# Kernel optimization log

Measured on AMD Instinct MI355X. Metric: run time of the kernel, lower is better.

## Reference

```python
import jax, jax.numpy as jnp
import numpy as np

B, S, D, H = 4, 1024, 768, 12
E = D // H  # head dim = 64

def setup_inputs() -> dict:
    key = jax.random.key(0)
    ks = jax.random.split(key, 8)
    sd = 1.0 / np.sqrt(D)
    return {
        'x':    jax.random.normal(ks[0], (B, S, D), jnp.float32),
        'Wqkv': jax.random.normal(ks[1], (3 * D, D), jnp.float32) * sd,
        'Wl':   jax.random.normal(ks[2], (H, H), jnp.float32) * (1.0 / np.sqrt(H)),
        'bl':   jax.random.normal(ks[3], (H,), jnp.float32) * 0.01,
        'Ww':   jax.random.normal(ks[4], (H, H), jnp.float32) * (1.0 / np.sqrt(H)),
        'bw':   jax.random.normal(ks[5], (H,), jnp.float32) * 0.01,
        'Wp':   jax.random.normal(ks[6], (D, D), jnp.float32) * sd,
        'bp':   jax.random.normal(ks[7], (D,), jnp.float32) * 0.01,
    }

def reference(x, Wqkv, Wl, bl, Ww, bw, Wp, bp):
    # qkv: [B,S,3D] -> [B,S,3,H,E] -> q,k,v each [B,H,S,E]
    qkv = jnp.einsum('bsd,fd->bsf', x, Wqkv)
    qkv = qkv.reshape(B, S, 3, H, E).transpose(2, 0, 3, 1, 4)
    q, k, v = qkv[0], qkv[1], qkv[2]
    # NOTE: source computes but never applies the 1/sqrt(E) scale; stay faithful.
    attn = jnp.einsum('bhqe,bhke->bhqk', q, k)            # [B,H,S,S]
    # talking-heads mix before softmax: Linear over head axis
    attn = jnp.einsum('bhqk,gh->bgqk', attn, Wl) + bl[None, :, None, None]
    attn = jax.nn.softmax(attn, axis=-1)
    # talking-heads mix after softmax
    attn = jnp.einsum('bhqk,gh->bgqk', attn, Ww) + bw[None, :, None, None]
    out = jnp.einsum('bhqk,bhke->bhqe', attn, v)          # [B,H,S,E]
    out = out.transpose(0, 2, 1, 3).reshape(B, S, D)      # b h s e -> b s (h e)
    return jnp.einsum('bsd,fd->bsf', out, Wp) + bp
```

## Files before the change

### kernel.cpp

```cpp
#include <hip/hip_runtime.h>
#include <math.h>


typedef _Float16 f16;
typedef __attribute__((ext_vector_type(8))) _Float16 f16x8;
typedef __attribute__((ext_vector_type(4))) _Float16 f16x4;
typedef __attribute__((ext_vector_type(2))) _Float16 f16x2;
typedef __attribute__((ext_vector_type(4))) float f32x4;
typedef __attribute__((ext_vector_type(2))) float f32x2;
typedef __attribute__((ext_vector_type(2))) unsigned u32x2;
typedef unsigned short u16;

__device__ __forceinline__ u16 f2h(float f) {
  f16 h = (f16)f;
  return __builtin_bit_cast(u16, h);
}
__device__ __forceinline__ unsigned pk2h(float a, float b) {
  return __builtin_bit_cast(unsigned, __builtin_amdgcn_cvt_pkrtz(a, b));
}
__device__ __forceinline__ float exp2_native(float x) {
  float r;
  asm("v_exp_f32 %0, %1" : "=v"(r) : "v"(x));
  return r;
}

__device__ __forceinline__ void async16(const void* g, void* l) {
  __builtin_amdgcn_global_load_lds(
      (const __attribute__((address_space(1))) unsigned int*)g,
      (__attribute__((address_space(3))) unsigned int*)l, 16, 0, 0);
}

#define MFMA_F16(a, b, c) __builtin_amdgcn_mfma_f32_16x16x32_f16((a), (b), (c), 0, 0, 0)
#define MFMA16(a, b, c) __builtin_amdgcn_mfma_f32_16x16x16f16((a), (b), (c), 0, 0, 0)

__global__ __launch_bounds__(256) void k_prep(const float* __restrict__ x,
                                              const float* __restrict__ Wqkv,
                                              const float* __restrict__ Wp,
                                              u16* __restrict__ xh,
                                              u16* __restrict__ wh,
                                              u16* __restrict__ wph) {
  const int blk = blockIdx.x, t = threadIdx.x;
  if (blk < 3072) {
    int i = blk * 256 + t;
    float4 v = ((const float4*)x)[i];
    ((ushort4*)xh)[i] = make_ushort4(f2h(v.x), f2h(v.y), f2h(v.z), f2h(v.w));
  } else if (blk < 4800) {
    int i = (blk - 3072) * 256 + t;
    float4 v = ((const float4*)Wqkv)[i];
    ((ushort4*)wh)[i] = make_ushort4(f2h(v.x), f2h(v.y), f2h(v.z), f2h(v.w));
  } else {
    int i = (blk - 4800) * 256 + t;
    float4 v = ((const float4*)Wp)[i];
    ((ushort4*)wph)[i] = make_ushort4(f2h(v.x), f2h(v.y), f2h(v.z), f2h(v.w));
  }
}

__global__ __launch_bounds__(256) void k_qkv(const u16* __restrict__ Axh,
                                             const u16* __restrict__ Bwh,
                                             u16* __restrict__ qkf,
                                             u16* __restrict__ vbuf) {
  __shared__ u16 smem[16384];
  u16* As = smem;
  u16* Bs = smem + 4096;
  const int t = threadIdx.x, lane = t & 63, wave = t >> 6;
  const int wm = wave >> 1, wn = wave & 1;
  const int quad = lane >> 4, l16 = lane & 15;
  const int pid = blockIdx.x;
  const int group = pid / 144;
  const int rem = pid - group * 144;
  const int m0 = (group * 8 + (rem & 7)) * 128;
  const int n0 = (rem >> 3) * 128;
  const bool vblk = (n0 >= 1536);
  const int srow = t >> 2, sch = (t & 3) * 8;
  f32x4 acc[4][4];
#pragma unroll
  for (int i = 0; i < 4; ++i)
#pragma unroll
    for (int j = 0; j < 4; ++j) acc[i][j] = (f32x4){0.f, 0.f, 0.f, 0.f};
  for (int k0 = 0; k0 < 768; k0 += 32) {
    const size_t ga = (size_t)(m0 + srow) * 768 + k0 + sch;
    const size_t gb = (size_t)(n0 + srow) * 768 + k0 + sch;
    __syncthreads();
    async16(Axh + ga, &As[t * 8]);
    async16(Axh + ga + (size_t)64 * 768, &As[2048 + t * 8]);
    async16(Bwh + gb, &Bs[t * 8]);
    async16(Bwh + gb + (size_t)64 * 768, &Bs[2048 + t * 8]);
    __syncthreads();
    f16x8 af[4], bfr[4];
#pragma unroll
    for (int i = 0; i < 4; ++i) af[i] = *(const f16x8*)&As[(wm * 64 + i * 16 + l16) * 32 + quad * 8];
#pragma unroll
    for (int j = 0; j < 4; ++j) bfr[j] = *(const f16x8*)&Bs[(wn * 64 + j * 16 + l16) * 32 + quad * 8];
#pragma unroll
    for (int i = 0; i < 4; ++i)
#pragma unroll
      for (int j = 0; j < 4; ++j) acc[i][j] = MFMA_F16(af[i], bfr[j], acc[i][j]);
  }
  __syncthreads();
  u16* T = smem;
#pragma unroll
  for (int i = 0; i < 4; ++i)
#pragma unroll
    for (int j = 0; j < 4; ++j)
#pragma unroll
      for (int r = 0; r < 4; ++r) {
        const int row = wm * 64 + i * 16 + quad * 4 + r;
        const int col = wn * 64 + j * 16 + l16;
        T[row * 128 + (col ^ ((row & 7) << 4))] = f2h(acc[i][j][r]);
      }
  __syncthreads();
  const int row = t >> 1, halfc = (t & 1) * 64;
  const int sw = (row & 7) << 4;
  u16* dst = vblk ? (vbuf + (size_t)(m0 + row) * 768 + (n0 - 1536) + halfc)
                  : (qkf + (size_t)(m0 + row) * 1536 + n0 + halfc);
#pragma unroll
  for (int c = 0; c < 64; c += 8)
    *(uint4*)(dst + c) = *(const uint4*)&T[row * 128 + ((halfc + c) ^ sw)];
}

__global__ __launch_bounds__(256) void k_qk(const u16* __restrict__ qkf,
                                            u16* __restrict__ scbuf) {
  __shared__ u16 smem[17408];
  u16* As = smem;
  u16* Bs = smem + 8192;
  const int t = threadIdx.x, lane = t & 63, wave = t >> 6;
  const int wm = wave >> 1, wn = wave & 1;
  const int quad = lane >> 4, l16 = lane & 15;
  const int bh = blockIdx.z, b = bh / 12, h = bh % 12;
  const int m0 = blockIdx.y * 128, n0 = blockIdx.x * 128;
#pragma unroll
  for (int i = 0; i < 4; ++i) {
    const int ci = i * 256 + t;
    const int row = ci >> 3, ch = ci & 7;
    const int chs = ch ^ (row & 7);
    async16(qkf + (size_t)(b * 1024 + m0 + row) * 1536 + h * 64 + chs * 8, &As[ci * 8]);
    async16(qkf + (size_t)(b * 1024 + n0 + row) * 1536 + 768 + h * 64 + chs * 8, &Bs[ci * 8]);
  }
  f32x4 acc[4][4];
#pragma unroll
  for (int i = 0; i < 4; ++i)
#pragma unroll
    for (int j = 0; j < 4; ++j) acc[i][j] = (f32x4){0.f, 0.f, 0.f, 0.f};
  __syncthreads();
  const int sx = l16 & 7;
#pragma unroll
  for (int k0 = 0; k0 < 2; ++k0) {
    const int fch = ((k0 * 4 + quad) ^ sx) * 8;
    f16x8 af[4], bfr[4];
#pragma unroll
    for (int i = 0; i < 4; ++i) af[i] = *(const f16x8*)&As[(wm * 64 + i * 16 + l16) * 64 + fch];
#pragma unroll
    for (int j = 0; j < 4; ++j) bfr[j] = *(const f16x8*)&Bs[(wn * 64 + j * 16 + l16) * 64 + fch];
#pragma unroll
    for (int i = 0; i < 4; ++i)
#pragma unroll
      for (int j = 0; j < 4; ++j) acc[i][j] = MFMA_F16(af[i], bfr[j], acc[i][j]);
  }
  __syncthreads();
  u16* T = smem;
#pragma unroll
  for (int i = 0; i < 4; ++i)
#pragma unroll
    for (int j = 0; j < 4; ++j)
#pragma unroll
      for (int r = 0; r < 4; ++r) {
        const int row = wm * 64 + i * 16 + quad * 4 + r;
        const int col = wn * 64 + j * 16 + l16;
        T[row * 136 + col] = f2h(acc[i][j][r]);
      }
  __syncthreads();
  const int row = t >> 1, halfc = (t & 1) * 64;
  u16* dst = scbuf + ((size_t)(b * 1024 + m0 + row) * 12 + h) * 1024 + n0 + halfc;
#pragma unroll
  for (int c = 0; c < 64; c += 8)
    *(uint4*)(dst + c) = *(const uint4*)&T[row * 136 + halfc + c];
}

__global__ __launch_bounds__(256) void k_mix(u16* __restrict__ scbuf,
                                             const float* __restrict__ Wl,
                                             const float* __restrict__ bl,
                                             const float* __restrict__ Ww,
                                             const float* __restrict__ bw) {
  __shared__ float red[4][16];
  const int t = threadIdx.x, lane = t & 63, wave = t >> 6;
  const int quad = lane >> 4, l16 = lane & 15;
  const int bq = blockIdx.x, b = bq >> 10, q = bq & 1023;
  const size_t qslab = (size_t)(b * 1024 + q) * 12288;
  const float L2E = 1.44269504088896f;
  const bool actA = (quad < 3);
  f16x4 Awl = (f16x4){0, 0, 0, 0}, Aww = (f16x4){0, 0, 0, 0};
  if (actA && l16 < 12) {
    const float4 wl4 = *(const float4*)&Wl[l16 * 12 + quad * 4];
    const float4 ww4 = *(const float4*)&Ww[l16 * 12 + quad * 4];
    Awl[0] = (f16)(wl4.x * L2E); Awl[1] = (f16)(wl4.y * L2E);
    Awl[2] = (f16)(wl4.z * L2E); Awl[3] = (f16)(wl4.w * L2E);
    Aww[0] = (f16)ww4.x; Aww[1] = (f16)ww4.y; Aww[2] = (f16)ww4.z; Aww[3] = (f16)ww4.w;
  }
  float blv[4], bwv[4];
#pragma unroll
  for (int r = 0; r < 4; ++r) {
    blv[r] = actA ? (bl[quad * 4 + r] - 16.f) * L2E : 0.f;
    bwv[r] = actA ? bw[quad * 4 + r] : 0.f;
  }
  const u16* const Sg = scbuf + qslab + (size_t)(quad * 4) * 1024 + l16;
  float Ev[16][4];
  float a0 = 0.f, a1 = 0.f, a2 = 0.f, a3 = 0.f;
#pragma unroll
  for (int i = 0; i < 16; ++i) {
    const int kb = (wave * 16 + i) * 16;
    f16x4 B1 = (f16x4){0, 0, 0, 0};
    if (actA) {
#pragma unroll
      for (int j = 0; j < 4; ++j) B1[j] = __builtin_bit_cast(f16, Sg[j * 1024 + kb]);
    }
    f32x4 c1 = (f32x4){blv[0], blv[1], blv[2], blv[3]};
    c1 = MFMA16(Awl, B1, c1);
    const float e0 = exp2_native(c1[0]), e1 = exp2_native(c1[1]);
    const float e2 = exp2_native(c1[2]), e3 = exp2_native(c1[3]);
    Ev[i][0] = e0; Ev[i][1] = e1; Ev[i][2] = e2; Ev[i][3] = e3;
    a0 += e0; a1 += e1; a2 += e2; a3 += e3;
  }
#pragma unroll
  for (int m = 1; m <= 8; m <<= 1) {
    a0 += __shfl_xor(a0, m); a1 += __shfl_xor(a1, m);
    a2 += __shfl_xor(a2, m); a3 += __shfl_xor(a3, m);
  }
  if (l16 == 0) {
    red[wave][quad * 4 + 0] = a0; red[wave][quad * 4 + 1] = a1;
    red[wave][quad * 4 + 2] = a2; red[wave][quad * 4 + 3] = a3;
  }
  __syncthreads();
  float dinv[4];
#pragma unroll
  for (int r = 0; r < 4; ++r) {
    const int g = quad * 4 + r;
    dinv[r] = 1.0f / (red[0][g] + red[1][g] + red[2][g] + red[3][g]);
  }
  u16* const outp = scbuf + qslab + (size_t)quad * 4096 + l16;
#pragma unroll
  for (int i = 0; i < 16; ++i) {
    const int kb = (wave * 16 + i) * 16;
    const unsigned lo = pk2h(Ev[i][0] * dinv[0], Ev[i][1] * dinv[1]);
    const unsigned hi = pk2h(Ev[i][2] * dinv[2], Ev[i][3] * dinv[3]);
    u32x2 pw = {lo, hi};
    const f16x4 Pf = __builtin_bit_cast(f16x4, pw);
    f32x4 c2 = (f32x4){bwv[0], bwv[1], bwv[2], bwv[3]};
    c2 = MFMA16(Aww, Pf, c2);
    if (actA) {
#pragma unroll
      for (int r = 0; r < 4; ++r) outp[r * 1024 + kb] = f2h(c2[r]);
    }
  }
}

__global__ __launch_bounds__(256) void k_pv(const u16* __restrict__ probs,
                                            const u16* __restrict__ vbuf,
                                            u16* __restrict__ ctx) {
  __shared__ u16 As[4096];
  __shared__ u16 Bs[64 * 40];
  const int t = threadIdx.x, lane = t & 63, wave = t >> 6;
  const int wm = wave >> 1, wn = wave & 1;
  const int quad = lane >> 4, l16 = lane & 15;
  const int bh = blockIdx.y, b = bh / 12, h = bh % 12;
  const int m0 = blockIdx.x * 128;
  const int srow = t >> 2, sch = (t & 3) * 8;
  const int ev = t & 63, s8 = (t >> 6) * 8;
  f32x4 acc[4][2];
#pragma unroll
  for (int i = 0; i < 4; ++i)
#pragma unroll
    for (int j = 0; j < 2; ++j) acc[i][j] = (f32x4){0.f, 0.f, 0.f, 0.f};
  for (int k0 = 0; k0 < 1024; k0 += 32) {
    const u16* vp = vbuf + (size_t)(b * 1024 + k0 + s8) * 768 + h * 64 + ev;
    u16 vcol[8];
#pragma unroll
    for (int i = 0; i < 8; ++i) vcol[i] = vp[(size_t)i * 768];
    __syncthreads();
    const u16* ga = probs + ((size_t)(b * 1024 + m0 + srow) * 12 + h) * 1024 + k0 + sch;
    async16(ga, &As[t * 8]);
    async16(ga + (size_t)64 * 12 * 1024, &As[2048 + t * 8]);
    *(ushort4*)&Bs[ev * 40 + s8] = make_ushort4(vcol[0], vcol[1], vcol[2], vcol[3]);
    *(ushort4*)&Bs[ev * 40 + s8 + 4] = make_ushort4(vcol[4], vcol[5], vcol[6], vcol[7]);
    __syncthreads();
    f16x8 af[4], bfr[2];
#pragma unroll
    for (int i = 0; i < 4; ++i) af[i] = *(const f16x8*)&As[(wm * 64 + i * 16 + l16) * 32 + quad * 8];
#pragma unroll
    for (int j = 0; j < 2; ++j) bfr[j] = *(const f16x8*)&Bs[(wn * 32 + j * 16 + l16) * 40 + quad * 8];
#pragma unroll
    for (int i = 0; i < 4; ++i)
#pragma unroll
      for (int j = 0; j < 2; ++j) acc[i][j] = MFMA_F16(af[i], bfr[j], acc[i][j]);
  }
#pragma unroll
  for (int i = 0; i < 4; ++i)
#pragma unroll
    for (int j = 0; j < 2; ++j)
#pragma unroll
      for (int r = 0; r < 4; ++r) {
        int q = m0 + wm * 64 + i * 16 + quad * 4 + r;
        int e = wn * 32 + j * 16 + l16;
        ctx[(size_t)(b * 1024 + q) * 768 + h * 64 + e] = f2h(acc[i][j][r]);
      }
}

__global__ __launch_bounds__(256) void k_oproj(const u16* __restrict__ A,
                                               const u16* __restrict__ Bm,
                                               const float* __restrict__ bp,
                                               float* __restrict__ out) {
  __shared__ u16 As[4096];
  __shared__ u16 Bs[4096];
  const int t = threadIdx.x, lane = t & 63, wave = t >> 6;
  const int wm = wave >> 1, wn = wave & 1;
  const int quad = lane >> 4, l16 = lane & 15;
  const int m0 = blockIdx.y * 128, n0 = blockIdx.x * 128;
  const int srow = t >> 2, sch = (t & 3) * 8;
  f32x4 acc[4][4];
#pragma unroll
  for (int i = 0; i < 4; ++i)
#pragma unroll
    for (int j = 0; j < 4; ++j) acc[i][j] = (f32x4){0.f, 0.f, 0.f, 0.f};
  for (int k0 = 0; k0 < 768; k0 += 32) {
    __syncthreads();
    const u16* ga = A + (size_t)(m0 + srow) * 768 + k0 + sch;
    const u16* gb = Bm + (size_t)(n0 + srow) * 768 + k0 + sch;
    async16(ga, &As[t * 8]);
    async16(ga + (size_t)64 * 768, &As[2048 + t * 8]);
    async16(gb, &Bs[t * 8]);
    async16(gb + (size_t)64 * 768, &Bs[2048 + t * 8]);
    __syncthreads();
    f16x8 af[4], bfr[4];
#pragma unroll
    for (int i = 0; i < 4; ++i) af[i] = *(const f16x8*)&As[(wm * 64 + i * 16 + l16) * 32 + quad * 8];
#pragma unroll
    for (int j = 0; j < 4; ++j) bfr[j] = *(const f16x8*)&Bs[(wn * 64 + j * 16 + l16) * 32 + quad * 8];
#pragma unroll
    for (int i = 0; i < 4; ++i)
#pragma unroll
      for (int j = 0; j < 4; ++j) acc[i][j] = MFMA_F16(af[i], bfr[j], acc[i][j]);
  }
#pragma unroll
  for (int i = 0; i < 4; ++i)
#pragma unroll
    for (int j = 0; j < 4; ++j)
#pragma unroll
      for (int r = 0; r < 4; ++r) {
        const int row = m0 + wm * 64 + i * 16 + quad * 4 + r;
        const int col = n0 + wn * 64 + j * 16 + l16;
        out[(size_t)row * 768 + col] = acc[i][j][r] + bp[col];
      }
}

extern "C" void kernel_launch(void* const* d_in, const int* in_sizes, int n_in,
                              void* d_out, int out_size, void* d_ws, size_t ws_size,
                              hipStream_t stream) {
  const float* x    = (const float*)d_in[0];
  const float* Wqkv = (const float*)d_in[1];
  const float* Wl   = (const float*)d_in[2];
  const float* bl   = (const float*)d_in[3];
  const float* Ww   = (const float*)d_in[4];
  const float* bw   = (const float*)d_in[5];
  const float* Wp   = (const float*)d_in[6];
  const float* bp   = (const float*)d_in[7];
  float* out = (float*)d_out;

  char* ws = (char*)d_ws;
  u16* scbuf = (u16*)(ws + 0);
  u16* qkf   = (u16*)(ws + 100663296ull);
  u16* vbuf  = (u16*)(ws + 113246208ull);
  u16* ctx   = (u16*)(ws + 119537664ull);
  u16* x_h   = (u16*)(ws + 125829120ull);
  u16* wq_h  = (u16*)(ws + 132120576ull);
  u16* wp_h  = (u16*)(ws + 135659520ull);

  hipLaunchKernelGGL(k_prep, dim3(5376), dim3(256), 0, stream,
                     x, Wqkv, Wp, x_h, wq_h, wp_h);
  hipLaunchKernelGGL(k_qkv,  dim3(576),      dim3(256), 0, stream, x_h, wq_h, qkf, vbuf);
  hipLaunchKernelGGL(k_qk,   dim3(8, 8, 48), dim3(256), 0, stream, qkf, scbuf);
  hipLaunchKernelGGL(k_mix,  dim3(4096),     dim3(256), 0, stream, scbuf, Wl, bl, Ww, bw);
  hipLaunchKernelGGL(k_pv,   dim3(8, 48),    dim3(256), 0, stream, scbuf, vbuf, ctx);
  hipLaunchKernelGGL(k_oproj, dim3(6, 32),   dim3(256), 0, stream, ctx, wp_h, bp, out);
}
```

Measured before the change: 242.8 us.

## Process two query rows per mix block and retile PV with swizzled LDS

```diff
diff --git a/kernel.cpp b/kernel.cpp
--- a/kernel.cpp
+++ b/kernel.cpp
@@ -181,11 +181,11 @@
                                              const float* __restrict__ bl,
                                              const float* __restrict__ Ww,
                                              const float* __restrict__ bw) {
-  __shared__ float red[4][16];
-  const int t = threadIdx.x, lane = t & 63, wave = t >> 6;
-  const int quad = lane >> 4, l16 = lane & 15;
-  const int bq = blockIdx.x, b = bq >> 10, q = bq & 1023;
-  const size_t qslab = (size_t)(b * 1024 + q) * 12288;
+  __shared__ float red[2][4][16];
+  const int t = threadIdx.x, lane = t & 63, wave = t >> 6;
+  const int quad = lane >> 4, l16 = lane & 15;
+  const int pr = blockIdx.x, b = pr >> 9, q0 = (pr & 511) * 2;
+  const size_t qslab = (size_t)(b * 1024 + q0) * 12288;
   const float L2E = 1.44269504088896f;
   const bool actA = (quad < 3);
   f16x4 Awl = (f16x4){0, 0, 0, 0}, Aww = (f16x4){0, 0, 0, 0};
@@ -202,53 +202,77 @@
     blv[r] = actA ? (bl[quad * 4 + r] - 16.f) * L2E : 0.f;
     bwv[r] = actA ? bw[quad * 4 + r] : 0.f;
   }
-  const u16* const Sg = scbuf + qslab + (size_t)(quad * 4) * 1024 + l16;
-  float Ev[16][4];
-  float a0 = 0.f, a1 = 0.f, a2 = 0.f, a3 = 0.f;
+  const u16* const Sg0 = scbuf + qslab + (size_t)(quad * 4) * 1024 + l16;
+  const u16* const Sg1 = Sg0 + 12288;
+  float Ev0[16][4], Ev1[16][4];
+  float s0[4] = {0.f, 0.f, 0.f, 0.f}, s1[4] = {0.f, 0.f, 0.f, 0.f};
 #pragma unroll
   for (int i = 0; i < 16; ++i) {
     const int kb = (wave * 16 + i) * 16;
-    f16x4 B1 = (f16x4){0, 0, 0, 0};
+    f16x4 B0 = (f16x4){0, 0, 0, 0}, B1 = (f16x4){0, 0, 0, 0};
     if (actA) {
 #pragma unroll
-      for (int j = 0; j < 4; ++j) B1[j] = __builtin_bit_cast(f16, Sg[j * 1024 + kb]);
-    }
-    f32x4 c1 = (f32x4){blv[0], blv[1], blv[2], blv[3]};
+      for (int j = 0; j < 4; ++j) {
+        B0[j] = __builtin_bit_cast(f16, Sg0[j * 1024 + kb]);
+        B1[j] = __builtin_bit_cast(f16, Sg1[j * 1024 + kb]);
+      }
+    }
+    f32x4 c0 = (f32x4){blv[0], blv[1], blv[2], blv[3]};
+    f32x4 c1 = c0;
+    c0 = MFMA16(Awl, B0, c0);
     c1 = MFMA16(Awl, B1, c1);
-    const float e0 = exp2_native(c1[0]), e1 = exp2_native(c1[1]);
-    const float e2 = exp2_native(c1[2]), e3 = exp2_native(c1[3]);
-    Ev[i][0] = e0; Ev[i][1] = e1; Ev[i][2] = e2; Ev[i][3] = e3;
-    a0 += e0; a1 += e1; a2 += e2; a3 += e3;
+#pragma unroll
+    for (int r = 0; r < 4; ++r) {
+      const float e0 = exp2_native(c0[r]);
+      const float e1 = exp2_native(c1[r]);
+      Ev0[i][r] = e0; Ev1[i][r] = e1;
+      s0[r] += e0; s1[r] += e1;
+    }
   }
 #pragma unroll
   for (int m = 1; m <= 8; m <<= 1) {
-    a0 += __shfl_xor(a0, m); a1 += __shfl_xor(a1, m);
-    a2 += __shfl_xor(a2, m); a3 += __shfl_xor(a3, m);
+#pragma unroll
+    for (int r = 0; r < 4; ++r) {
+      s0[r] += __shfl_xor(s0[r], m);
+      s1[r] += __shfl_xor(s1[r], m);
+    }
   }
   if (l16 == 0) {
-    red[wave][quad * 4 + 0] = a0; red[wave][quad * 4 + 1] = a1;
-    red[wave][quad * 4 + 2] = a2; red[wave][quad * 4 + 3] = a3;
-  }
-  __syncthreads();
-  float dinv[4];
+#pragma unroll
+    for (int r = 0; r < 4; ++r) {
+      red[0][wave][quad * 4 + r] = s0[r];
+      red[1][wave][quad * 4 + r] = s1[r];
+    }
+  }
+  __syncthreads();
+  float dinv0[4], dinv1[4];
 #pragma unroll
   for (int r = 0; r < 4; ++r) {
     const int g = quad * 4 + r;
-    dinv[r] = 1.0f / (red[0][g] + red[1][g] + red[2][g] + red[3][g]);
-  }
-  u16* const outp = scbuf + qslab + (size_t)quad * 4096 + l16;
+    dinv0[r] = 1.0f / (red[0][0][g] + red[0][1][g] + red[0][2][g] + red[0][3][g]);
+    dinv1[r] = 1.0f / (red[1][0][g] + red[1][1][g] + red[1][2][g] + red[1][3][g]);
+  }
+  u16* const outp0 = scbuf + qslab + (size_t)quad * 4096 + l16;
+  u16* const outp1 = outp0 + 12288;
 #pragma unroll
   for (int i = 0; i < 16; ++i) {
     const int kb = (wave * 16 + i) * 16;
-    const unsigned lo = pk2h(Ev[i][0] * dinv[0], Ev[i][1] * dinv[1]);
-    const unsigned hi = pk2h(Ev[i][2] * dinv[2], Ev[i][3] * dinv[3]);
-    u32x2 pw = {lo, hi};
-    const f16x4 Pf = __builtin_bit_cast(f16x4, pw);
-    f32x4 c2 = (f32x4){bwv[0], bwv[1], bwv[2], bwv[3]};
-    c2 = MFMA16(Aww, Pf, c2);
+    u32x2 pw0 = {pk2h(Ev0[i][0] * dinv0[0], Ev0[i][1] * dinv0[1]),
+                 pk2h(Ev0[i][2] * dinv0[2], Ev0[i][3] * dinv0[3])};
+    u32x2 pw1 = {pk2h(Ev1[i][0] * dinv1[0], Ev1[i][1] * dinv1[1]),
+                 pk2h(Ev1[i][2] * dinv1[2], Ev1[i][3] * dinv1[3])};
+    const f16x4 P0 = __builtin_bit_cast(f16x4, pw0);
+    const f16x4 P1 = __builtin_bit_cast(f16x4, pw1);
+    f32x4 c20 = (f32x4){bwv[0], bwv[1], bwv[2], bwv[3]};
+    f32x4 c21 = c20;
+    c20 = MFMA16(Aww, P0, c20);
+    c21 = MFMA16(Aww, P1, c21);
     if (actA) {
 #pragma unroll
-      for (int r = 0; r < 4; ++r) outp[r * 1024 + kb] = f2h(c2[r]);
+      for (int r = 0; r < 4; ++r) {
+        outp0[r * 1024 + kb] = f2h(c20[r]);
+        outp1[r * 1024 + kb] = f2h(c21[r]);
+      }
     }
   }
 }
@@ -256,52 +280,44 @@
 __global__ __launch_bounds__(256) void k_pv(const u16* __restrict__ probs,
                                             const u16* __restrict__ vbuf,
                                             u16* __restrict__ ctx) {
-  __shared__ u16 As[4096];
+  __shared__ u16 As[2048];
   __shared__ u16 Bs[64 * 40];
   const int t = threadIdx.x, lane = t & 63, wave = t >> 6;
-  const int wm = wave >> 1, wn = wave & 1;
   const int quad = lane >> 4, l16 = lane & 15;
   const int bh = blockIdx.y, b = bh / 12, h = bh % 12;
-  const int m0 = blockIdx.x * 128;
-  const int srow = t >> 2, sch = (t & 3) * 8;
+  const int m0 = blockIdx.x * 64;
+  const int prow = t >> 2, pchs = (t & 3) ^ (prow & 3);
   const int ev = t & 63, s8 = (t >> 6) * 8;
-  f32x4 acc[4][2];
-#pragma unroll
-  for (int i = 0; i < 4; ++i)
-#pragma unroll
-    for (int j = 0; j < 2; ++j) acc[i][j] = (f32x4){0.f, 0.f, 0.f, 0.f};
+  const int fch = (quad ^ (l16 & 3)) * 8;
+  f32x4 acc[4];
+#pragma unroll
+  for (int j = 0; j < 4; ++j) acc[j] = (f32x4){0.f, 0.f, 0.f, 0.f};
   for (int k0 = 0; k0 < 1024; k0 += 32) {
     const u16* vp = vbuf + (size_t)(b * 1024 + k0 + s8) * 768 + h * 64 + ev;
     u16 vcol[8];
 #pragma unroll
     for (int i = 0; i < 8; ++i) vcol[i] = vp[(size_t)i * 768];
     __syncthreads();
-    const u16* ga = probs + ((size_t)(b * 1024 + m0 + srow) * 12 + h) * 1024 + k0 + sch;
-    async16(ga, &As[t * 8]);
-    async16(ga + (size_t)64 * 12 * 1024, &As[2048 + t * 8]);
+    async16(probs + ((size_t)(b * 1024 + m0 + prow) * 12 + h) * 1024 + k0 + pchs * 8,
+            &As[t * 8]);
     *(ushort4*)&Bs[ev * 40 + s8] = make_ushort4(vcol[0], vcol[1], vcol[2], vcol[3]);
     *(ushort4*)&Bs[ev * 40 + s8 + 4] = make_ushort4(vcol[4], vcol[5], vcol[6], vcol[7]);
     __syncthreads();
-    f16x8 af[4], bfr[2];
-#pragma unroll
-    for (int i = 0; i < 4; ++i) af[i] = *(const f16x8*)&As[(wm * 64 + i * 16 + l16) * 32 + quad * 8];
-#pragma unroll
-    for (int j = 0; j < 2; ++j) bfr[j] = *(const f16x8*)&Bs[(wn * 32 + j * 16 + l16) * 40 + quad * 8];
-#pragma unroll
-    for (int i = 0; i < 4; ++i)
-#pragma unroll
-      for (int j = 0; j < 2; ++j) acc[i][j] = MFMA_F16(af[i], bfr[j], acc[i][j]);
-  }
-#pragma unroll
-  for (int i = 0; i < 4; ++i)
-#pragma unroll
-    for (int j = 0; j < 2; ++j)
-#pragma unroll
-      for (int r = 0; r < 4; ++r) {
-        int q = m0 + wm * 64 + i * 16 + quad * 4 + r;
-        int e = wn * 32 + j * 16 + l16;
-        ctx[(size_t)(b * 1024 + q) * 768 + h * 64 + e] = f2h(acc[i][j][r]);
-      }
+    f16x8 af = *(const f16x8*)&As[(wave * 16 + l16) * 32 + fch];
+    f16x8 bfr[4];
+#pragma unroll
+    for (int j = 0; j < 4; ++j) bfr[j] = *(const f16x8*)&Bs[(j * 16 + l16) * 40 + quad * 8];
+#pragma unroll
+    for (int j = 0; j < 4; ++j) acc[j] = MFMA_F16(af, bfr[j], acc[j]);
+  }
+#pragma unroll
+  for (int j = 0; j < 4; ++j)
+#pragma unroll
+    for (int r = 0; r < 4; ++r) {
+      const int q = m0 + wave * 16 + quad * 4 + r;
+      const int e = j * 16 + l16;
+      ctx[(size_t)(b * 1024 + q) * 768 + h * 64 + e] = f2h(acc[j][r]);
+    }
 }
 
 __global__ __launch_bounds__(256) void k_oproj(const u16* __restrict__ A,
@@ -377,7 +393,7 @@
                      x, Wqkv, Wp, x_h, wq_h, wp_h);
   hipLaunchKernelGGL(k_qkv,  dim3(576),      dim3(256), 0, stream, x_h, wq_h, qkf, vbuf);
   hipLaunchKernelGGL(k_qk,   dim3(8, 8, 48), dim3(256), 0, stream, qkf, scbuf);
-  hipLaunchKernelGGL(k_mix,  dim3(4096),     dim3(256), 0, stream, scbuf, Wl, bl, Ww, bw);
-  hipLaunchKernelGGL(k_pv,   dim3(8, 48),    dim3(256), 0, stream, scbuf, vbuf, ctx);
+  hipLaunchKernelGGL(k_mix,  dim3(2048),     dim3(256), 0, stream, scbuf, Wl, bl, Ww, bw);
+  hipLaunchKernelGGL(k_pv,   dim3(16, 48),   dim3(256), 0, stream, scbuf, vbuf, ctx);
   hipLaunchKernelGGL(k_oproj, dim3(6, 32),   dim3(256), 0, stream, ctx, wp_h, bp, out);
 }
```

After: 249.8 us. 2.9% more time.
